# Optimization experiments

Hardware: AMD Instinct MI355X
Metric: run time of the kernel (lower is better)

Reference implementation:

```python
import jax, jax.numpy as jnp
import numpy as np
from jax import lax


def _quadrature_weights(bw):
    # s2cnn-style Driscoll-Healy quadrature weights over beta, length 2*bw
    j = np.arange(2 * bw)
    k = np.arange(bw)
    theta = np.pi * (2 * j + 1) / (4 * bw)
    s = (np.sin(np.outer(2 * j + 1, 2 * k + 1) * np.pi / (4 * bw)) / (2 * k + 1)).sum(-1)
    return jnp.asarray((2.0 / bw) * np.sin(theta) * s, jnp.float32)


def _conv2d(x, W, b):
    y = lax.conv_general_dilated(x, W, (1, 1), 'SAME',
                                 dimension_numbers=('NCHW', 'OIHW', 'NCHW'))
    return y + b[None, :, None, None]


def setup_inputs() -> dict:
    key = jax.random.key(0)
    ks = jax.random.split(key, 8)
    b, n = 8, 32768
    res_pt, res_r = 32, 8
    inputs = jax.random.normal(ks[0], (b, n, 3), jnp.float32)
    return {
        'inputs': inputs,
        'scale': jnp.float32(3.0),      # max radius covered by radial bins
        'sigma': jnp.float32(0.5),      # gaussian width in grid units
        'A': jnp.float32(1.0),          # splat amplitude
        'inteval_comp': jnp.float32(0.5),
        'res_pt': res_pt,
        'res_r': res_r,
        'W_s2_1': 0.08 * jax.random.normal(ks[1], (32, 8, 3, 3), jnp.float32),
        'b_s2_1': jnp.zeros((32,), jnp.float32),
        'W_s2_2': 0.05 * jax.random.normal(ks[2], (64, 32, 3, 3), jnp.float32),
        'b_s2_2': jnp.zeros((64,), jnp.float32),
        'W_gamma': 0.1 * jax.random.normal(ks[3], (64, 32), jnp.float32),
        'W_c3_1': 0.05 * jax.random.normal(ks[4], (64, 128), jnp.float32),
        'b_c3_1': jnp.zeros((64,), jnp.float32),
        'W_c3_2': 0.05 * jax.random.normal(ks[5], (32, 64), jnp.float32),
        'b_c3_2': jnp.zeros((32,), jnp.float32),
    }


def reference(inputs, scale, sigma, A, inteval_comp, res_pt, res_r,
              W_s2_1, b_s2_1, W_s2_2, b_s2_2, W_gamma,
              W_c3_1, b_c3_1, W_c3_2, b_c3_2):
    b, n, _ = inputs.shape
    # ---- remap: cartesian -> spherical with min-radius clamp (utils.remap) ----
    x, y, z = inputs[..., 0], inputs[..., 1], inputs[..., 2]
    r = jnp.maximum(jnp.sqrt(x * x + y * y + z * z), 0.1)
    theta = jnp.arccos(jnp.clip(z / r, -1.0, 1.0))            # [0, pi]
    phi = jnp.arctan2(y, x) + np.pi                            # [0, 2pi)
    # ---- s2_gridding: gaussian-weighted point -> (theta,phi,r) grid scatter ----
    ct = theta / np.pi * res_pt                                # continuous bin coords
    cp = phi / (2 * np.pi) * res_pt
    cr = r / scale * res_r
    it = jnp.clip(jnp.floor(ct).astype(jnp.int32), 0, res_pt - 1)
    ip = jnp.clip(jnp.floor(cp).astype(jnp.int32), 0, res_pt - 1)
    ir = jnp.clip(jnp.floor(cr).astype(jnp.int32), 0, res_r - 1)
    d2 = ((ct - (it + inteval_comp)) ** 2
          + (cp - (ip + inteval_comp)) ** 2
          + (cr - (ir + inteval_comp)) ** 2)
    w = A * jnp.exp(-d2 / (2.0 * sigma * sigma))               # (b, n)
    vals = jnp.stack([w, w * x, w * y, w * z], axis=-1)        # (b, n, 4)
    bidx = jnp.arange(b, dtype=jnp.int32)[:, None] * jnp.ones((1, n), jnp.int32)
    flat = ((bidx * res_pt + it) * res_pt + ip) * res_r + ir   # (b, n)
    grid = jnp.zeros((b * res_pt * res_pt * res_r, 4), jnp.float32)
    grid = grid.at[flat.reshape(-1)].add(vals.reshape(-1, 4))
    grid = grid.reshape(b, res_pt, res_pt, res_r, 4)
    ft = jnp.transpose(grid[..., 0], (0, 3, 1, 2))             # (b, res_r, res_pt, res_pt)
    # ---- encoder_l1 (s2cnn_equators): S2 convs + gamma lift to SO3 grid ----
    h = jax.nn.relu(_conv2d(ft, W_s2_1, b_s2_1))
    h = jax.nn.relu(_conv2d(h, W_s2_2, b_s2_2))                # (b, 64, res_pt, res_pt)
    ft_grid = jnp.einsum('bcxy,cg->bcxyg', h, W_gamma)         # (b, 64, rp, rp, rp)
    # ---- so3_integrate: quadrature weight over beta, sum alpha/gamma ----
    wq = _quadrature_weights(res_pt // 2)                      # (res_pt,)
    ft_max = jnp.einsum('bcxyg,y->bc', ft_grid, wq)            # (b, 64)
    # ---- broadcast global feature, concat, pointwise conv3d head ----
    ft_max_ = jnp.broadcast_to(ft_max[:, :, None, None, None],
                               (b, ft_grid.shape[1], res_pt, res_pt, res_pt))
    cat = jnp.concatenate([ft_grid, ft_max_], axis=1)          # (b, 128, rp, rp, rp)
    h3 = jax.nn.relu(jnp.einsum('bcxyg,dc->bdxyg', cat, W_c3_1)
                     + b_c3_1[None, :, None, None, None])
    out = (jnp.einsum('bdxyg,ed->bexyg', h3, W_c3_2)
           + b_c3_2[None, :, None, None, None])                # (b, 32, rp, rp, rp)
    ft_g = out.reshape(b, out.shape[1], -1).max(-1)            # (b, 32)
    return (out, ft_g)
```

## Files before the change

kernel.cpp:

```cpp
#include <hip/hip_runtime.h>
#include <math.h>

#define PI_D 3.14159265358979323846
#define PI_F 3.14159265358979323846f

typedef _Float16 half8 __attribute__((ext_vector_type(8)));
typedef _Float16 half4v __attribute__((ext_vector_type(4)));
typedef float floatx4 __attribute__((ext_vector_type(4)));
#define MFMA16(a,b,c) __builtin_amdgcn_mfma_f32_16x16x32_f16(a,b,c,0,0,0)

__global__ void k_prep(const float* __restrict__ Wg, const float* __restrict__ Wc31,
                       const float* __restrict__ Wc32,
                       _Float16* __restrict__ VswH, _Float16* __restrict__ VswL,
                       _Float16* __restrict__ W2swH, _Float16* __restrict__ W2swL,
                       float* __restrict__ ft, float* __restrict__ WS,
                       float* __restrict__ wq, float* __restrict__ sgs) {
  int flat = blockIdx.x * 256 + threadIdx.x;
  {
    int jj = flat & 7;
    int l  = (flat >> 3) & 63;
    int rest = flat >> 9;
    int ks = rest & 1, mt = rest >> 1;
    int c = ks*32 + (l >> 4)*8 + jj;
    int m = mt*16 + (l & 15);
    int g = m >> 6, d = m & 63;
    float val = Wg[c*32 + g] * Wc31[d*128 + c];
    _Float16 hi = (_Float16)val;
    VswH[flat] = hi;
    VswL[flat] = (_Float16)(val - (float)hi);
  }
  if (flat < 2048) {
    int jj = flat & 7;
    int l  = (flat >> 3) & 63;
    int rest = flat >> 9;
    int ks = rest & 1, mt2 = rest >> 1;
    int e = mt2*16 + (l & 15);
    int d = ks*32 + (l >> 4)*8 + jj;
    float val = Wc32[e*64 + d];
    _Float16 hi = (_Float16)val;
    W2swH[flat] = hi;
    W2swL[flat] = (_Float16)(val - (float)hi);
  }
  if (flat < 16384) ((float4*)ft)[flat] = make_float4(0.f, 0.f, 0.f, 0.f);
  if (flat < 32) {
    double jj = 2.0*(double)flat + 1.0;
    double theta = PI_D * jj / 64.0;
    double s = 0.0;
    for (int k = 0; k < 16; ++k)
      s += sin(jj * (double)(2*k+1) * PI_D / 64.0) / (double)(2*k+1);
    wq[flat] = (float)((2.0/16.0) * sin(theta) * s);
  } else if (flat < 96) {
    int c = flat - 32;
    float s = 0.f;
    for (int g = 0; g < 32; ++g) s += Wg[c*32 + g];
    sgs[c] = s;
  } else if (flat < 608) {
    WS[flat - 96] = 0.f;
  }
}

__global__ void k_scatter(const float* __restrict__ inp,
                          const float* __restrict__ p_scale,
                          const float* __restrict__ p_sigma,
                          const float* __restrict__ p_A,
                          const float* __restrict__ p_ic,
                          float* __restrict__ ft) {
  int i = blockIdx.x * 256 + threadIdx.x;
  float scale = p_scale[0];
  float sigma = p_sigma[0];
  float A     = p_A[0];
  float icomp = p_ic[0];
  int b = i >> 15;
  float x = inp[i*3+0];
  float y = inp[i*3+1];
  float z = inp[i*3+2];
  float r = sqrtf(x*x + y*y + z*z);
  r = fmaxf(r, 0.1f);
  float ctv = fminf(fmaxf(z / r, -1.0f), 1.0f);
  float theta = acosf(ctv);
  float phi = atan2f(y, x) + PI_F;
  float ct = theta * (32.0f / PI_F);
  float cp = phi * (32.0f / (2.0f * PI_F));
  float cr = r / scale * 8.0f;
  int it = (int)floorf(ct); it = min(max(it, 0), 31);
  int ip = (int)floorf(cp); ip = min(max(ip, 0), 31);
  int ir = (int)floorf(cr); ir = min(max(ir, 0), 7);
  float dt = ct - ((float)it + icomp);
  float dp = cp - ((float)ip + icomp);
  float dr = cr - ((float)ir + icomp);
  float d2 = dt*dt + dp*dp + dr*dr;
  float w = A * expf(-d2 / (2.0f * sigma * sigma));
  atomicAdd(&ft[((b*8 + ir)*32 + it)*32 + ip], w);
}

__global__ void k_conv1(const float* __restrict__ ft, const float* __restrict__ W,
                        const float* __restrict__ bias, float* __restrict__ h1) {
  int blk = blockIdx.x;
  int b = blk >> 5, oc = blk & 31;
  __shared__ float Ws[72];
  int t = threadIdx.x;
  if (t < 72) Ws[t] = W[oc*72 + t];
  __syncthreads();
  int x = t >> 5, y = t & 31;
  float acc = bias[oc];
  const float* fb = ft + b*8192;
  for (int ic = 0; ic < 8; ++ic) {
    const float* fc = fb + ic*1024;
    const float* wr = Ws + ic*9;
#pragma unroll
    for (int dx = -1; dx <= 1; ++dx) {
      int xx = x + dx;
      bool okx = ((unsigned)xx < 32u);
#pragma unroll
      for (int dy = -1; dy <= 1; ++dy) {
        int yy = y + dy;
        float v = (okx && ((unsigned)yy < 32u)) ? fc[xx*32 + yy] : 0.f;
        acc = fmaf(v, wr[(dx+1)*3 + (dy+1)], acc);
      }
    }
  }
  h1[(b*32 + oc)*1024 + t] = fmaxf(acc, 0.f);
}

__global__ __launch_bounds__(512) void k_conv2(const float* __restrict__ h1,
                        const float* __restrict__ W,
                        const float* __restrict__ bias,
                        const float* __restrict__ wq,
                        float* __restrict__ h2, float* __restrict__ WS) {
  int blk = blockIdx.x;
  int b = blk >> 5, q = blk & 31;
  int oc0 = (q >> 1) * 4, xh = q & 1;
  __shared__ float Ws[4*288];
  int t = threadIdx.x;
  for (int idx = t; idx < 4*288; idx += 512) Ws[idx] = W[oc0*288 + idx];
  __syncthreads();
  int x = xh*16 + (t >> 5), y = t & 31;
  float a0 = bias[oc0+0], a1 = bias[oc0+1], a2 = bias[oc0+2], a3 = bias[oc0+3];
  const float* hb = h1 + b*32*1024;
  for (int ic = 0; ic < 32; ++ic) {
    const float* hc = hb + ic*1024;
    const float* w0 = Ws + 0*288 + ic*9;
    const float* w1 = Ws + 1*288 + ic*9;
    const float* w2 = Ws + 2*288 + ic*9;
    const float* w3 = Ws + 3*288 + ic*9;
#pragma unroll
    for (int dx = -1; dx <= 1; ++dx) {
      int xx = x + dx;
      bool okx = ((unsigned)xx < 32u);
#pragma unroll
      for (int dy = -1; dy <= 1; ++dy) {
        int yy = y + dy;
        float v = (okx && ((unsigned)yy < 32u)) ? hc[xx*32 + yy] : 0.f;
        int k = (dx+1)*3 + (dy+1);
        a0 = fmaf(v, w0[k], a0);
        a1 = fmaf(v, w1[k], a1);
        a2 = fmaf(v, w2[k], a2);
        a3 = fmaf(v, w3[k], a3);
      }
    }
  }
  float r0 = fmaxf(a0, 0.f), r1 = fmaxf(a1, 0.f);
  float r2 = fmaxf(a2, 0.f), r3 = fmaxf(a3, 0.f);
  int pp = x*32 + y;
  h2[(b*64 + oc0+0)*1024 + pp] = r0;
  h2[(b*64 + oc0+1)*1024 + pp] = r1;
  h2[(b*64 + oc0+2)*1024 + pp] = r2;
  h2[(b*64 + oc0+3)*1024 + pp] = r3;
  float wqv = wq[y];
  float s0 = r0*wqv, s1 = r1*wqv, s2 = r2*wqv, s3 = r3*wqv;
#pragma unroll
  for (int m = 1; m < 64; m <<= 1) {
    s0 += __shfl_xor(s0, m, 64);
    s1 += __shfl_xor(s1, m, 64);
    s2 += __shfl_xor(s2, m, 64);
    s3 += __shfl_xor(s3, m, 64);
  }
  if ((t & 63) == 0) {
    atomicAdd(&WS[b*64 + oc0+0], s0);
    atomicAdd(&WS[b*64 + oc0+1], s1);
    atomicAdd(&WS[b*64 + oc0+2], s2);
    atomicAdd(&WS[b*64 + oc0+3], s3);
  }
}

__global__ __launch_bounds__(512, 4) void k_head(
    const float* __restrict__ h2, const float* __restrict__ WS,
    const float* __restrict__ sgs,
    const float* __restrict__ Wc31, const float* __restrict__ bc31,
    const float* __restrict__ bc32,
    const half8* __restrict__ VswH, const half8* __restrict__ VswL,
    const half8* __restrict__ W2swH, const half8* __restrict__ W2swL,
    float* __restrict__ out, float* __restrict__ blockmax) {
  __shared__ __align__(16) _Float16 h3H[512*72];
  __shared__ float Ks[64];
  __shared__ float vbuf2[128];
  int blk = blockIdx.x;
  int b = blk >> 6, x = (blk >> 1) & 31, h = blk & 1;
  int t = threadIdx.x;
  int lane = t & 63, w = t >> 6;
  int n16 = lane & 15, quad = lane >> 4;

  if (t < 64) {
    float acc = bc31[t];
    const float* wr = Wc31 + t*128 + 64;
    const float* wsb = WS + b*64;
    for (int c = 0; c < 64; ++c)
      acc = fmaf(wr[c], sgs[c]*wsb[c], acc);
    Ks[t] = acc;
  }

  half8 bh00, bh01, bh10, bh11, bl00, bl01, bl10, bl11;
  {
    const float* h2b = h2 + (size_t)b*64*1024 + x*32;
#pragma unroll
    for (int j = 0; j < 8; ++j) {
      int c0 = quad*8 + j;
      int c1 = 32 + c0;
      float f00 = h2b[c0*1024 + n16];
      float f01 = h2b[c1*1024 + n16];
      float f10 = h2b[c0*1024 + 16 + n16];
      float f11 = h2b[c1*1024 + 16 + n16];
      _Float16 g00 = (_Float16)f00, g01 = (_Float16)f01;
      _Float16 g10 = (_Float16)f10, g11 = (_Float16)f11;
      bh00[j] = g00;  bl00[j] = (_Float16)(f00 - (float)g00);
      bh01[j] = g01;  bl01[j] = (_Float16)(f01 - (float)g01);
      bh10[j] = g10;  bl10[j] = (_Float16)(f10 - (float)g10);
      bh11[j] = g11;  bl11[j] = (_Float16)(f11 - (float)g11);
    }
  }
  int mt2 = w & 1;
  half8 a2h0 = W2swH[(mt2*2 + 0)*64 + lane];
  half8 a2h1 = W2swH[(mt2*2 + 1)*64 + lane];
  half8 a2l0 = W2swL[(mt2*2 + 0)*64 + lane];
  half8 a2l1 = W2swL[(mt2*2 + 1)*64 + lane];
  float bias_e[4];
#pragma unroll
  for (int r = 0; r < 4; ++r) bias_e[r] = bc32[mt2*16 + quad*4 + r];
  __syncthreads();

  for (int i = 0; i < 8; ++i) {
    int mt = h*64 + w*8 + i;
    half8 ah0 = VswH[(mt*2 + 0)*64 + lane];
    half8 ah1 = VswH[(mt*2 + 1)*64 + lane];
    half8 al0 = VswL[(mt*2 + 0)*64 + lane];
    half8 al1 = VswL[(mt*2 + 1)*64 + lane];
    floatx4 acc0 = {0.f, 0.f, 0.f, 0.f};
    floatx4 acc1 = {0.f, 0.f, 0.f, 0.f};
    acc0 = MFMA16(ah0, bh00, acc0);  acc1 = MFMA16(ah0, bh10, acc1);
    acc0 = MFMA16(ah0, bl00, acc0);  acc1 = MFMA16(ah0, bl10, acc1);
    acc0 = MFMA16(al0, bh00, acc0);  acc1 = MFMA16(al0, bh10, acc1);
    acc0 = MFMA16(ah1, bh01, acc0);  acc1 = MFMA16(ah1, bh11, acc1);
    acc0 = MFMA16(ah1, bl01, acc0);  acc1 = MFMA16(ah1, bl11, acc1);
    acc0 = MFMA16(al1, bh01, acc0);  acc1 = MFMA16(al1, bh11, acc1);
    int g = mt >> 2, gl = g & 15;
    int dbase = (mt & 3)*16 + quad*4;
    float4 kv = *(const float4*)&Ks[dbase];
#pragma unroll
    for (int nt = 0; nt < 2; ++nt) {
      floatx4 a = nt ? acc1 : acc0;
      int y = nt*16 + n16;
      int rowc = y*16 + gl;
      int dsw = (dbase + y*8) & 63;
      half4v hv;
      hv[0] = (_Float16)fmaxf(a[0] + kv.x, 0.f);
      hv[1] = (_Float16)fmaxf(a[1] + kv.y, 0.f);
      hv[2] = (_Float16)fmaxf(a[2] + kv.z, 0.f);
      hv[3] = (_Float16)fmaxf(a[3] + kv.w, 0.f);
      *(half4v*)&h3H[rowc*72 + dsw] = hv;
    }
  }
  __syncthreads();
  float vmax[4] = {-3.4e38f, -3.4e38f, -3.4e38f, -3.4e38f};
  for (int i = 0; i < 8; ++i) {
    int nt2 = (w >> 1)*8 + i;
    int rowc = nt2*16 + n16;
    int dsw0 = (quad*8 + nt2*8) & 63;
    int dsw1 = (32 + quad*8 + nt2*8) & 63;
    half8 b2h0 = *(const half8*)&h3H[rowc*72 + dsw0];
    half8 b2h1 = *(const half8*)&h3H[rowc*72 + dsw1];
    floatx4 acc = {0.f, 0.f, 0.f, 0.f};
    acc = MFMA16(a2h0, b2h0, acc);
    acc = MFMA16(a2l0, b2h0, acc);
    acc = MFMA16(a2h1, b2h1, acc);
    acc = MFMA16(a2l1, b2h1, acc);
    int y = nt2, g = h*16 + n16;
    size_t base = (((size_t)(b*32 + mt2*16 + quad*4))*1024 + (size_t)(x*32 + y))*32 + g;
#pragma unroll
    for (int r = 0; r < 4; ++r) {
      float v = acc[r] + bias_e[r];
      out[base + (size_t)r*32768] = v;
      vmax[r] = fmaxf(vmax[r], v);
    }
  }
#pragma unroll
  for (int m = 1; m < 16; m <<= 1) {
#pragma unroll
    for (int r = 0; r < 4; ++r)
      vmax[r] = fmaxf(vmax[r], __shfl_xor(vmax[r], m, 64));
  }
  if (n16 == 0) {
#pragma unroll
    for (int r = 0; r < 4; ++r) vbuf2[w*16 + quad*4 + r] = vmax[r];
  }
  __syncthreads();
  if (t < 32) {
    int e = t, m2 = e >> 4, el = e & 15;
    float mm = fmaxf(fmaxf(vbuf2[(m2+0)*16 + el], vbuf2[(m2+2)*16 + el]),
                     fmaxf(vbuf2[(m2+4)*16 + el], vbuf2[(m2+6)*16 + el]));
    blockmax[blk*32 + e] = mm;
  }
}

__global__ void k_final(const float* __restrict__ blockmax, float* __restrict__ ftg) {
  int t = threadIdx.x;
  int b = t >> 5, e = t & 31;
  float m = -3.4e38f;
  for (int s = 0; s < 64; ++s) m = fmaxf(m, blockmax[(b*64 + s)*32 + e]);
  ftg[b*32 + e] = m;
}

extern "C" void kernel_launch(void* const* d_in, const int* in_sizes, int n_in,
                              void* d_out, int out_size, void* d_ws, size_t ws_size,
                              hipStream_t stream) {
  const float* inputs = (const float*)d_in[0];
  const float* scale  = (const float*)d_in[1];
  const float* sigma  = (const float*)d_in[2];
  const float* A      = (const float*)d_in[3];
  const float* icmp   = (const float*)d_in[4];
  const float* W1   = (const float*)d_in[7];
  const float* b1   = (const float*)d_in[8];
  const float* W2   = (const float*)d_in[9];
  const float* b2   = (const float*)d_in[10];
  const float* Wg   = (const float*)d_in[11];
  const float* Wc31 = (const float*)d_in[12];
  const float* bc31 = (const float*)d_in[13];
  const float* Wc32 = (const float*)d_in[14];
  const float* bc32 = (const float*)d_in[15];

  float* ws    = (float*)d_ws;
  float* ft    = ws;
  float* h1    = ws + 65536;
  float* h2    = ws + 327680;
  float* WS    = ws + 851968;
  float* bmax  = ws + 852480;
  float* wq    = ws + 868864;
  float* sgs   = ws + 868896;
  _Float16* VswH  = (_Float16*)(ws + 868960);
  _Float16* VswL  = (_Float16*)(ws + 934496);
  _Float16* W2swH = (_Float16*)(ws + 1000032);
  _Float16* W2swL = (_Float16*)(ws + 1001056);
  float* out   = (float*)d_out;
  float* ftg   = out + 8388608;

  k_prep<<<512, 256, 0, stream>>>(Wg, Wc31, Wc32, VswH, VswL, W2swH, W2swL,
                                  ft, WS, wq, sgs);
  k_scatter<<<1024, 256, 0, stream>>>(inputs, scale, sigma, A, icmp, ft);
  k_conv1<<<256, 1024, 0, stream>>>(ft, W1, b1, h1);
  k_conv2<<<256, 512, 0, stream>>>(h1, W2, b2, wq, h2, WS);
  k_head<<<512, 512, 0, stream>>>(h2, WS, sgs, Wc31, bc31, bc32,
                                  (const half8*)VswH, (const half8*)VswL,
                                  (const half8*)W2swH, (const half8*)W2swL,
                                  out, bmax);
  k_final<<<1, 256, 0, stream>>>(bmax, ftg);
}
```

Before: 186.1 us.

## Fuse conv1 and conv2 per row with halo recompute; fold final max into head

```diff
diff --git a/kernel.cpp b/kernel.cpp
--- a/kernel.cpp
+++ b/kernel.cpp
@@ -14,7 +14,8 @@
                        _Float16* __restrict__ VswH, _Float16* __restrict__ VswL,
                        _Float16* __restrict__ W2swH, _Float16* __restrict__ W2swL,
                        float* __restrict__ ft, float* __restrict__ WS,
-                       float* __restrict__ wq, float* __restrict__ sgs) {
+                       float* __restrict__ wq, float* __restrict__ sgs,
+                       int* __restrict__ ticket) {
   int flat = blockIdx.x * 256 + threadIdx.x;
   {
     int jj = flat & 7;
@@ -56,6 +57,8 @@
     sgs[c] = s;
   } else if (flat < 608) {
     WS[flat - 96] = 0.f;
+  } else if (flat == 608) {
+    *ticket = 0;
   }
 }
 
@@ -93,93 +96,123 @@
   atomicAdd(&ft[((b*8 + ir)*32 + it)*32 + ip], w);
 }
 
-__global__ void k_conv1(const float* __restrict__ ft, const float* __restrict__ W,
-                        const float* __restrict__ bias, float* __restrict__ h1) {
+__global__ __launch_bounds__(512) void k_conv12(
+    const float* __restrict__ ft, const float* __restrict__ W1,
+    const float* __restrict__ b1, const float* __restrict__ W2,
+    const float* __restrict__ b2, const float* __restrict__ wq,
+    float* __restrict__ h2, float* __restrict__ WS) {
+  __shared__ __align__(16) float ftt[8][5][32];
+  __shared__ __align__(16) float h1t[32][3][32];
+  __shared__ __align__(16) float W1s[72*32];
+  __shared__ __align__(16) float W2s[288*64];
   int blk = blockIdx.x;
-  int b = blk >> 5, oc = blk & 31;
-  __shared__ float Ws[72];
+  int b = blk >> 5, xt = blk & 31;
   int t = threadIdx.x;
-  if (t < 72) Ws[t] = W[oc*72 + t];
-  __syncthreads();
-  int x = t >> 5, y = t & 31;
-  float acc = bias[oc];
-  const float* fb = ft + b*8192;
-  for (int ic = 0; ic < 8; ++ic) {
-    const float* fc = fb + ic*1024;
-    const float* wr = Ws + ic*9;
-#pragma unroll
-    for (int dx = -1; dx <= 1; ++dx) {
-      int xx = x + dx;
-      bool okx = ((unsigned)xx < 32u);
-#pragma unroll
-      for (int dy = -1; dy <= 1; ++dy) {
-        int yy = y + dy;
-        float v = (okx && ((unsigned)yy < 32u)) ? fc[xx*32 + yy] : 0.f;
-        acc = fmaf(v, wr[(dx+1)*3 + (dy+1)], acc);
+
+  for (int idx = t; idx < 2304; idx += 512) {
+    int oc2 = idx & 31, rest = idx >> 5;
+    W1s[rest*32 + oc2] = W1[oc2*72 + rest];
+  }
+  for (int idx = t; idx < 18432; idx += 512) {
+    int oc = idx & 63, rest = idx >> 6;
+    W2s[rest*64 + oc] = W2[oc*288 + rest];
+  }
+  for (int idx = t; idx < 1280; idx += 512) {
+    int y = idx & 31, xx = (idx >> 5) % 5, ic = idx / 160;
+    int xg = xt + xx - 2;
+    ftt[ic][xx][y] = ((unsigned)xg < 32u) ? ft[b*8192 + ic*1024 + xg*32 + y] : 0.f;
+  }
+  __syncthreads();
+
+  {
+    int y = t & 31, grp = t >> 5;
+    float acc[2][3];
+    float bb0 = b1[grp*2+0], bb1 = b1[grp*2+1];
+#pragma unroll
+    for (int xr = 0; xr < 3; ++xr) { acc[0][xr] = bb0; acc[1][xr] = bb1; }
+    for (int ic = 0; ic < 8; ++ic) {
+      float v[5][3];
+#pragma unroll
+      for (int dyi = 0; dyi < 3; ++dyi) {
+        int yy = y + dyi - 1;
+        bool ok = ((unsigned)yy < 32u);
+        int yc = min(max(yy, 0), 31);
+#pragma unroll
+        for (int xx = 0; xx < 5; ++xx) {
+          float tv = ftt[ic][xx][yc];
+          v[xx][dyi] = ok ? tv : 0.f;
+        }
       }
-    }
-  }
-  h1[(b*32 + oc)*1024 + t] = fmaxf(acc, 0.f);
-}
-
-__global__ __launch_bounds__(512) void k_conv2(const float* __restrict__ h1,
-                        const float* __restrict__ W,
-                        const float* __restrict__ bias,
-                        const float* __restrict__ wq,
-                        float* __restrict__ h2, float* __restrict__ WS) {
-  int blk = blockIdx.x;
-  int b = blk >> 5, q = blk & 31;
-  int oc0 = (q >> 1) * 4, xh = q & 1;
-  __shared__ float Ws[4*288];
-  int t = threadIdx.x;
-  for (int idx = t; idx < 4*288; idx += 512) Ws[idx] = W[oc0*288 + idx];
-  __syncthreads();
-  int x = xh*16 + (t >> 5), y = t & 31;
-  float a0 = bias[oc0+0], a1 = bias[oc0+1], a2 = bias[oc0+2], a3 = bias[oc0+3];
-  const float* hb = h1 + b*32*1024;
-  for (int ic = 0; ic < 32; ++ic) {
-    const float* hc = hb + ic*1024;
-    const float* w0 = Ws + 0*288 + ic*9;
-    const float* w1 = Ws + 1*288 + ic*9;
-    const float* w2 = Ws + 2*288 + ic*9;
-    const float* w3 = Ws + 3*288 + ic*9;
-#pragma unroll
-    for (int dx = -1; dx <= 1; ++dx) {
-      int xx = x + dx;
-      bool okx = ((unsigned)xx < 32u);
-#pragma unroll
-      for (int dy = -1; dy <= 1; ++dy) {
-        int yy = y + dy;
-        float v = (okx && ((unsigned)yy < 32u)) ? hc[xx*32 + yy] : 0.f;
-        int k = (dx+1)*3 + (dy+1);
-        a0 = fmaf(v, w0[k], a0);
-        a1 = fmaf(v, w1[k], a1);
-        a2 = fmaf(v, w2[k], a2);
-        a3 = fmaf(v, w3[k], a3);
+#pragma unroll
+      for (int k = 0; k < 9; ++k) {
+        float2 w = *(const float2*)&W1s[(ic*9 + k)*32 + grp*2];
+        int dx = k / 3, dy = k % 3;
+#pragma unroll
+        for (int xr = 0; xr < 3; ++xr) {
+          float vv = v[xr + dx][dy];
+          acc[0][xr] = fmaf(vv, w.x, acc[0][xr]);
+          acc[1][xr] = fmaf(vv, w.y, acc[1][xr]);
+        }
       }
     }
-  }
-  float r0 = fmaxf(a0, 0.f), r1 = fmaxf(a1, 0.f);
-  float r2 = fmaxf(a2, 0.f), r3 = fmaxf(a3, 0.f);
-  int pp = x*32 + y;
-  h2[(b*64 + oc0+0)*1024 + pp] = r0;
-  h2[(b*64 + oc0+1)*1024 + pp] = r1;
-  h2[(b*64 + oc0+2)*1024 + pp] = r2;
-  h2[(b*64 + oc0+3)*1024 + pp] = r3;
-  float wqv = wq[y];
-  float s0 = r0*wqv, s1 = r1*wqv, s2 = r2*wqv, s3 = r3*wqv;
-#pragma unroll
-  for (int m = 1; m < 64; m <<= 1) {
-    s0 += __shfl_xor(s0, m, 64);
-    s1 += __shfl_xor(s1, m, 64);
-    s2 += __shfl_xor(s2, m, 64);
-    s3 += __shfl_xor(s3, m, 64);
-  }
-  if ((t & 63) == 0) {
-    atomicAdd(&WS[b*64 + oc0+0], s0);
-    atomicAdd(&WS[b*64 + oc0+1], s1);
-    atomicAdd(&WS[b*64 + oc0+2], s2);
-    atomicAdd(&WS[b*64 + oc0+3], s3);
+#pragma unroll
+    for (int xr = 0; xr < 3; ++xr) {
+      int xg = xt + xr - 1;
+      bool ok = ((unsigned)xg < 32u);
+      h1t[grp*2+0][xr][y] = ok ? fmaxf(acc[0][xr], 0.f) : 0.f;
+      h1t[grp*2+1][xr][y] = ok ? fmaxf(acc[1][xr], 0.f) : 0.f;
+    }
+  }
+  __syncthreads();
+
+  {
+    int y = t & 31, og = t >> 5, oc0 = og*4;
+    float a0 = b2[oc0+0], a1 = b2[oc0+1], a2 = b2[oc0+2], a3 = b2[oc0+3];
+    for (int ic2 = 0; ic2 < 32; ++ic2) {
+      float v[3][3];
+#pragma unroll
+      for (int dyi = 0; dyi < 3; ++dyi) {
+        int yy = y + dyi - 1;
+        bool ok = ((unsigned)yy < 32u);
+        int yc = min(max(yy, 0), 31);
+#pragma unroll
+        for (int xxi = 0; xxi < 3; ++xxi) {
+          float tv = h1t[ic2][xxi][yc];
+          v[xxi][dyi] = ok ? tv : 0.f;
+        }
+      }
+#pragma unroll
+      for (int k = 0; k < 9; ++k) {
+        float4 w = *(const float4*)&W2s[(ic2*9 + k)*64 + oc0];
+        float vv = v[k/3][k%3];
+        a0 = fmaf(vv, w.x, a0);
+        a1 = fmaf(vv, w.y, a1);
+        a2 = fmaf(vv, w.z, a2);
+        a3 = fmaf(vv, w.w, a3);
+      }
+    }
+    float r0 = fmaxf(a0, 0.f), r1 = fmaxf(a1, 0.f);
+    float r2 = fmaxf(a2, 0.f), r3 = fmaxf(a3, 0.f);
+    int pp = xt*32 + y;
+    h2[(b*64 + oc0+0)*1024 + pp] = r0;
+    h2[(b*64 + oc0+1)*1024 + pp] = r1;
+    h2[(b*64 + oc0+2)*1024 + pp] = r2;
+    h2[(b*64 + oc0+3)*1024 + pp] = r3;
+    float wqv = wq[y];
+    float s0 = r0*wqv, s1 = r1*wqv, s2 = r2*wqv, s3 = r3*wqv;
+#pragma unroll
+    for (int m = 1; m < 32; m <<= 1) {
+      s0 += __shfl_xor(s0, m, 64);
+      s1 += __shfl_xor(s1, m, 64);
+      s2 += __shfl_xor(s2, m, 64);
+      s3 += __shfl_xor(s3, m, 64);
+    }
+    if ((t & 31) == 0) {
+      atomicAdd(&WS[b*64 + oc0+0], s0);
+      atomicAdd(&WS[b*64 + oc0+1], s1);
+      atomicAdd(&WS[b*64 + oc0+2], s2);
+      atomicAdd(&WS[b*64 + oc0+3], s3);
+    }
   }
 }
 
@@ -190,10 +223,12 @@
     const float* __restrict__ bc32,
     const half8* __restrict__ VswH, const half8* __restrict__ VswL,
     const half8* __restrict__ W2swH, const half8* __restrict__ W2swL,
-    float* __restrict__ out, float* __restrict__ blockmax) {
+    float* __restrict__ out, float* __restrict__ blockmax,
+    int* __restrict__ ticket, float* __restrict__ ftg) {
   __shared__ __align__(16) _Float16 h3H[512*72];
   __shared__ float Ks[64];
   __shared__ float vbuf2[128];
+  __shared__ int lastflag;
   int blk = blockIdx.x;
   int b = blk >> 6, x = (blk >> 1) & 31, h = blk & 1;
   int t = threadIdx.x;
@@ -309,14 +344,22 @@
                      fmaxf(vbuf2[(m2+4)*16 + el], vbuf2[(m2+6)*16 + el]));
     blockmax[blk*32 + e] = mm;
   }
-}
-
-__global__ void k_final(const float* __restrict__ blockmax, float* __restrict__ ftg) {
-  int t = threadIdx.x;
-  int b = t >> 5, e = t & 31;
-  float m = -3.4e38f;
-  for (int s = 0; s < 64; ++s) m = fmaxf(m, blockmax[(b*64 + s)*32 + e]);
-  ftg[b*32 + e] = m;
+  __threadfence();
+  __syncthreads();
+  if (t == 0) {
+    int old = atomicAdd(ticket, 1);
+    lastflag = (old == 511) ? 1 : 0;
+  }
+  __syncthreads();
+  if (lastflag) {
+    __threadfence();
+    if (t < 256) {
+      int bb = t >> 5, e = t & 31;
+      float m = -3.4e38f;
+      for (int s = 0; s < 64; ++s) m = fmaxf(m, blockmax[(bb*64 + s)*32 + e]);
+      ftg[bb*32 + e] = m;
+    }
+  }
 }
 
 extern "C" void kernel_launch(void* const* d_in, const int* in_sizes, int n_in,
@@ -339,27 +382,25 @@
 
   float* ws    = (float*)d_ws;
   float* ft    = ws;
-  float* h1    = ws + 65536;
   float* h2    = ws + 327680;
   float* WS    = ws + 851968;
   float* bmax  = ws + 852480;
   float* wq    = ws + 868864;
   float* sgs   = ws + 868896;
-  _Float16* VswH  = (_Float16*)(ws + 868960);
-  _Float16* VswL  = (_Float16*)(ws + 934496);
-  _Float16* W2swH = (_Float16*)(ws + 1000032);
-  _Float16* W2swL = (_Float16*)(ws + 1001056);
+  int*   tick  = (int*)(ws + 868960);
+  _Float16* VswH  = (_Float16*)(ws + 868992);
+  _Float16* VswL  = (_Float16*)(ws + 934528);
+  _Float16* W2swH = (_Float16*)(ws + 1000064);
+  _Float16* W2swL = (_Float16*)(ws + 1001088);
   float* out   = (float*)d_out;
   float* ftg   = out + 8388608;
 
   k_prep<<<512, 256, 0, stream>>>(Wg, Wc31, Wc32, VswH, VswL, W2swH, W2swL,
-                                  ft, WS, wq, sgs);
+                                  ft, WS, wq, sgs, tick);
   k_scatter<<<1024, 256, 0, stream>>>(inputs, scale, sigma, A, icmp, ft);
-  k_conv1<<<256, 1024, 0, stream>>>(ft, W1, b1, h1);
-  k_conv2<<<256, 512, 0, stream>>>(h1, W2, b2, wq, h2, WS);
+  k_conv12<<<256, 512, 0, stream>>>(ft, W1, b1, W2, b2, wq, h2, WS);
   k_head<<<512, 512, 0, stream>>>(h2, WS, sgs, Wc31, bc31, bc32,
                                   (const half8*)VswH, (const half8*)VswL,
                                   (const half8*)W2swH, (const half8*)W2swL,
-                                  out, bmax);
-  k_final<<<1, 256, 0, stream>>>(bmax, ftg);
+                                  out, bmax, tick, ftg);
 }
```

Result: slower. 270.3 us (+45.3%).
